# Kernel tuning notes

Hardware: AMD Instinct MI355X
Metric: run time of the kernel (lower is better)

## Reference

```python
import jax, jax.numpy as jnp
import numpy as np

N = 524288      # total nodes
B = 4096        # number of graphs (segments)
D = 128         # input_dim
H = 256         # nb_hidden


def setup_inputs() -> dict:
    key = jax.random.key(0)
    ks = jax.random.split(key, 10)
    X = jax.random.normal(ks[0], (N, D), jnp.float32)
    # sorted, contiguous, non-empty segment ids (pyg `batch` vector)
    batch = ((jnp.arange(N) * B) // N).astype(jnp.int32)
    s = 0.05
    W0 = jax.random.normal(ks[1], (D, H), jnp.float32) * s
    b0 = jnp.zeros((H,), jnp.float32)
    W1 = jax.random.normal(ks[2], (H, H), jnp.float32) * s
    b1 = jnp.zeros((H,), jnp.float32)
    W2 = jax.random.normal(ks[3], (H, H), jnp.float32) * s
    b2 = jnp.zeros((H,), jnp.float32)
    Wf = jax.random.normal(ks[4], (H, 1), jnp.float32) * s
    bf = jnp.zeros((1,), jnp.float32)
    return {"X": X, "W0": W0, "b0": b0, "W1": W1, "b1": b1,
            "W2": W2, "b2": b2, "Wf": Wf, "bf": bf, "batch": batch}


def reference(X, W0, b0, W1, b1, W2, b2, Wf, bf, batch):
    # MLP logits (nb_layers=3 hidden Linear+ReLU, then final Linear to 1)
    h = jax.nn.relu(X @ W0 + b0)
    h = jax.nn.relu(h @ W1 + b1)
    h = jax.nn.relu(h @ W2 + b2)
    logits = (h @ Wf + bf)[:, 0]                          # [N]

    # batched_softmax: exp -> segment add -> gather -> div (as in original)
    e = jnp.exp(logits)
    seg_sum = jax.ops.segment_sum(e, batch, num_segments=B)   # [B]
    probs = e / seg_sum[batch]                                # [N]

    # batched_sample: per-segment categorical sample via Gumbel-max
    skey = jax.random.key(42)
    u = jax.random.uniform(skey, (N,), jnp.float32, 1e-20, 1.0)
    g = -jnp.log(-jnp.log(u))
    score = jnp.log(probs) + g                                # [N]
    seg_max = jax.ops.segment_max(score, batch, num_segments=B)
    winner = jnp.where(score >= seg_max[batch], jnp.arange(N), -1)
    shifted_actions = jax.ops.segment_max(winner, batch, num_segments=B)  # global idx per segment [B]
    p = probs[shifted_actions]                                # [B]

    # get_batch_shift: start offset of each segment
    counts = jax.ops.segment_sum(jnp.ones((N,), jnp.int32), batch, num_segments=B)
    starts = jnp.concatenate([jnp.zeros((1,), jnp.int32), jnp.cumsum(counts)[:-1]])
    actions = shifted_actions - starts                        # [B] local index within graph
    return (p, actions, shifted_actions)
```

## Files before the change

kernel.cpp:

```cpp
#include <hip/hip_runtime.h>
#include <hip/hip_bf16.h>


#define NFULL 524288
#define BSEG  4096
#define SEGSZ 128
#define DIN   128
#define HID   256
#define MROWS 128
#define KPAD  264

typedef __bf16 bf16x8 __attribute__((ext_vector_type(8)));
typedef float  f32x4  __attribute__((ext_vector_type(4)));

__device__ __forceinline__ unsigned short f2bf(float f) {
  __hip_bfloat16 h = __float2bfloat16(f);
  return __builtin_bit_cast(unsigned short, h);
}

__global__ __launch_bounds__(256) void convert_weights(
    const float* __restrict__ W0, const float* __restrict__ W1,
    const float* __restrict__ W2,
    unsigned short* __restrict__ W0t, unsigned short* __restrict__ W1t,
    unsigned short* __restrict__ W2t) {
  const int tid = blockIdx.x * 256 + threadIdx.x;
  if (tid < 32768) {
    const int n = tid >> 7, k = tid & 127;
    W0t[tid] = f2bf(W0[k * 256 + n]);
  } else if (tid < 98304) {
    const int u = tid - 32768;
    const int n = u >> 8, k = u & 255;
    W1t[u] = f2bf(W1[k * 256 + n]);
  } else if (tid < 163840) {
    const int u = tid - 98304;
    const int n = u >> 8, k = u & 255;
    W2t[u] = f2bf(W2[k * 256 + n]);
  }
}


template<int K>
__device__ __forceinline__ void do_layer(
    const unsigned short* Abuf, const unsigned short* __restrict__ Wt,
    const float* __restrict__ bias, int wq, int wr, int lane,
    f32x4 (&acc)[4][4]) {
  const int l15 = lane & 15;
  const int q   = lane >> 4;
  #pragma unroll
  for (int ct = 0; ct < 4; ++ct) {
    const float4 bv4 = *(const float4*)&bias[wq * 64 + ct * 16 + q * 4];
    f32x4 c; c[0] = bv4.x; c[1] = bv4.y; c[2] = bv4.z; c[3] = bv4.w;
    #pragma unroll
    for (int rt = 0; rt < 4; ++rt) acc[ct][rt] = c;
  }
  const unsigned short* Wb = Wt + (wq * 64 + l15) * K + q * 8;
  const unsigned short* Ab = Abuf + (wr * 64 + l15) * KPAD + q * 8;
  #pragma unroll 2
  for (int k0 = 0; k0 < K; k0 += 32) {
    bf16x8 wv[4], rv[4];
    #pragma unroll
    for (int ct = 0; ct < 4; ++ct)
      wv[ct] = *(const bf16x8*)(Wb + ct * 16 * K + k0);
    #pragma unroll
    for (int rt = 0; rt < 4; ++rt)
      rv[rt] = *(const bf16x8*)(Ab + rt * 16 * KPAD + k0);
    #pragma unroll
    for (int ct = 0; ct < 4; ++ct)
      #pragma unroll
      for (int rt = 0; rt < 4; ++rt)
        acc[ct][rt] = __builtin_amdgcn_mfma_f32_16x16x32_bf16(
            wv[ct], rv[rt], acc[ct][rt], 0, 0, 0);
  }
}

__device__ __forceinline__ void writeback_relu(
    unsigned short* Abuf, int wq, int wr, int lane, const f32x4 (&acc)[4][4]) {
  const int l15 = lane & 15, q = lane >> 4;
  #pragma unroll
  for (int rt = 0; rt < 4; ++rt) {
    const int row = wr * 64 + rt * 16 + l15;
    #pragma unroll
    for (int ct = 0; ct < 4; ++ct) {
      const int col = wq * 64 + ct * 16 + q * 4;
      ushort4 p;
      p.x = f2bf(fmaxf(acc[ct][rt][0], 0.f));
      p.y = f2bf(fmaxf(acc[ct][rt][1], 0.f));
      p.z = f2bf(fmaxf(acc[ct][rt][2], 0.f));
      p.w = f2bf(fmaxf(acc[ct][rt][3], 0.f));
      *(ushort4*)&Abuf[row * KPAD + col] = p;
    }
  }
}

__device__ __forceinline__ void threefry2x32_42(unsigned x0, unsigned x1,
                                                unsigned& o0, unsigned& o1) {
  const unsigned ks0 = 0u, ks1 = 42u;
  const unsigned ks2 = ks0 ^ ks1 ^ 0x1BD11BDAu;
  x0 += ks0; x1 += ks1;
#define TF_R(r) { x0 += x1; x1 = (x1 << (r)) | (x1 >> (32 - (r))); x1 ^= x0; }
  TF_R(13) TF_R(15) TF_R(26) TF_R(6)   x0 += ks1; x1 += ks2 + 1u;
  TF_R(17) TF_R(29) TF_R(16) TF_R(24)  x0 += ks2; x1 += ks0 + 2u;
  TF_R(13) TF_R(15) TF_R(26) TF_R(6)   x0 += ks0; x1 += ks1 + 3u;
  TF_R(17) TF_R(29) TF_R(16) TF_R(24)  x0 += ks1; x1 += ks2 + 4u;
  TF_R(13) TF_R(15) TF_R(26) TF_R(6)   x0 += ks2; x1 += ks0 + 5u;
#undef TF_R
  o0 = x0; o1 = x1;
}

__global__ __launch_bounds__(512, 4) void mlp_fused(
    const float* __restrict__ X,
    const unsigned short* __restrict__ W0t,
    const unsigned short* __restrict__ W1t,
    const unsigned short* __restrict__ W2t,
    const float* __restrict__ b0, const float* __restrict__ b1,
    const float* __restrict__ b2,
    const float* __restrict__ Wf, const float* __restrict__ bfp,
    float* __restrict__ out) {
  __shared__ alignas(16) unsigned short Abuf[MROWS * KPAD];
  __shared__ float WfS[HID];
  __shared__ float Lpart[8][64];
  __shared__ float logit_sh[MROWS];
  __shared__ float red[2];
  __shared__ float smax_sh[2];
  __shared__ int   sidx_sh[2];
  const int tid  = threadIdx.x;
  const int lane = tid & 63;
  const int w    = tid >> 6;
  const int wq   = w & 3;
  const int wr   = w >> 2;
  const int l15  = lane & 15;
  const int q    = lane >> 4;
  const int seg  = blockIdx.x;
  const size_t row0 = (size_t)seg * MROWS;

  if (tid < HID) WfS[tid] = Wf[tid];

  #pragma unroll
  for (int it = 0; it < 8; ++it) {
    const int idx = tid + it * 512;
    const int r   = idx >> 5;
    const int k4  = (idx & 31) * 4;
    const float4 v = *(const float4*)&X[(row0 + r) * DIN + k4];
    ushort4 p;
    p.x = f2bf(v.x); p.y = f2bf(v.y); p.z = f2bf(v.z); p.w = f2bf(v.w);
    *(ushort4*)&Abuf[r * KPAD + k4] = p;
  }
  __syncthreads();

  f32x4 acc[4][4];
  do_layer<DIN>(Abuf, W0t, b0, wq, wr, lane, acc);
  __syncthreads();
  writeback_relu(Abuf, wq, wr, lane, acc);
  __syncthreads();
  do_layer<HID>(Abuf, W1t, b1, wq, wr, lane, acc);
  __syncthreads();
  writeback_relu(Abuf, wq, wr, lane, acc);
  __syncthreads();
  do_layer<HID>(Abuf, W2t, b2, wq, wr, lane, acc);

  {
    float part[4];
    #pragma unroll
    for (int rt = 0; rt < 4; ++rt) {
      float p = 0.f;
      #pragma unroll
      for (int ct = 0; ct < 4; ++ct) {
        const int col = wq * 64 + ct * 16 + q * 4;
        #pragma unroll
        for (int r = 0; r < 4; ++r)
          p = fmaf(fmaxf(acc[ct][rt][r], 0.f), WfS[col + r], p);
      }
      part[rt] = p;
    }
    #pragma unroll
    for (int rt = 0; rt < 4; ++rt) {
      part[rt] += __shfl_xor(part[rt], 16, 64);
      part[rt] += __shfl_xor(part[rt], 32, 64);
    }
    if (q == 0)
      #pragma unroll
      for (int rt = 0; rt < 4; ++rt) Lpart[w][rt * 16 + l15] = part[rt];
  }
  __syncthreads();
  if (tid < MROWS) {
    const int g = (tid >> 6) * 4;
    const int r = tid & 63;
    logit_sh[tid] = Lpart[g][r] + Lpart[g + 1][r] + Lpart[g + 2][r] +
                    Lpart[g + 3][r] + bfp[0];
  }
  __syncthreads();

  float e = 0.f, score = 0.f, prob = 0.f;
  if (tid < SEGSZ) {
    e = expf(logit_sh[tid]);
    float v = e;
    #pragma unroll
    for (int off = 32; off >= 1; off >>= 1) v += __shfl_xor(v, off, 64);
    if ((tid & 63) == 0) red[tid >> 6] = v;
  }
  __syncthreads();
  if (tid < SEGSZ) {
    const float S = red[0] + red[1];
    prob = e / S;
    unsigned o0, o1;
    threefry2x32_42(0u, (unsigned)(row0 + tid), o0, o1);
    const float f = __uint_as_float(0x3f800000u | (o0 >> 9)) - 1.0f;
    const float u = fmaxf(1e-20f, f + 1e-20f);
    const float g = -logf(-logf(u));
    score = logf(prob) + g;
    logit_sh[tid] = prob;
    float ms = score; int mi = tid;
    #pragma unroll
    for (int off = 1; off < 64; off <<= 1) {
      const float os = __shfl_xor(ms, off, 64);
      const int   oi = __shfl_xor(mi, off, 64);
      if (os > ms || (os == ms && oi > mi)) { ms = os; mi = oi; }
    }
    if ((tid & 63) == 0) { smax_sh[tid >> 6] = ms; sidx_sh[tid >> 6] = mi; }
  }
  __syncthreads();
  if (tid == 0) {
    const float s0 = smax_sh[0], s1 = smax_sh[1];
    const int   i0 = sidx_sh[0], i1 = sidx_sh[1];
    const int win = (s1 > s0 || (s1 == s0 && i1 > i0)) ? i1 : i0;
    out[seg]            = logit_sh[win];
    out[BSEG + seg]     = (float)win;
    out[2 * BSEG + seg] = (float)(row0 + win);
  }
}

extern "C" void kernel_launch(void* const* d_in, const int* in_sizes, int n_in,
                              void* d_out, int out_size, void* d_ws, size_t ws_size,
                              hipStream_t stream) {
  const float* X  = (const float*)d_in[0];
  const float* W0 = (const float*)d_in[1];
  const float* b0 = (const float*)d_in[2];
  const float* W1 = (const float*)d_in[3];
  const float* b1 = (const float*)d_in[4];
  const float* W2 = (const float*)d_in[5];
  const float* b2 = (const float*)d_in[6];
  const float* Wf = (const float*)d_in[7];
  const float* bf = (const float*)d_in[8];

  unsigned short* W0t = (unsigned short*)d_ws;
  unsigned short* W1t = W0t + 256 * 128;
  unsigned short* W2t = W1t + 256 * 256;
  float* out = (float*)d_out;

  convert_weights<<<640, 256, 0, stream>>>(W0, W1, W2, W0t, W1t, W2t);
  mlp_fused<<<BSEG, 512, 0, stream>>>(X, W0t, W1t, W2t, b0, b1, b2,
                                      Wf, bf, out);
}
```

Before: 656.4 us.

## Use 4 waves per block with 128x64 warp tiles and coalesced weight reads

The fused MLP kernel drops from 8 waves to 4 waves per 128-row block. Each wave now computes all 128 rows for a 64-column slice, so it holds 32 accumulators, and each weight fragment loaded from global memory feeds twice as many MFMAs. This cuts weight traffic through L2/global per block in half, at the cost of more registers per lane and fewer waves available to hide latency. The weight-conversion kernel also switches to coalesced reads with scattered writes.

```diff
diff --git a/kernel.cpp b/kernel.cpp
--- a/kernel.cpp
+++ b/kernel.cpp
@@ -25,16 +25,16 @@
     unsigned short* __restrict__ W2t) {
   const int tid = blockIdx.x * 256 + threadIdx.x;
   if (tid < 32768) {
-    const int n = tid >> 7, k = tid & 127;
-    W0t[tid] = f2bf(W0[k * 256 + n]);
+    const int k = tid >> 8, n = tid & 255;
+    W0t[n * 128 + k] = f2bf(W0[tid]);
   } else if (tid < 98304) {
     const int u = tid - 32768;
-    const int n = u >> 8, k = u & 255;
-    W1t[u] = f2bf(W1[k * 256 + n]);
+    const int k = u >> 8, n = u & 255;
+    W1t[n * 256 + k] = f2bf(W1[u]);
   } else if (tid < 163840) {
     const int u = tid - 98304;
-    const int n = u >> 8, k = u & 255;
-    W2t[u] = f2bf(W2[k * 256 + n]);
+    const int k = u >> 8, n = u & 255;
+    W2t[n * 256 + k] = f2bf(W2[u]);
   }
 }
 
@@ -42,46 +42,45 @@
 template<int K>
 __device__ __forceinline__ void do_layer(
     const unsigned short* Abuf, const unsigned short* __restrict__ Wt,
-    const float* __restrict__ bias, int wq, int wr, int lane,
-    f32x4 (&acc)[4][4]) {
+    const float* __restrict__ bias, int w, int lane, f32x4 (&acc)[4][8]) {
   const int l15 = lane & 15;
   const int q   = lane >> 4;
   #pragma unroll
   for (int ct = 0; ct < 4; ++ct) {
-    const float4 bv4 = *(const float4*)&bias[wq * 64 + ct * 16 + q * 4];
+    const float4 bv4 = *(const float4*)&bias[w * 64 + ct * 16 + q * 4];
     f32x4 c; c[0] = bv4.x; c[1] = bv4.y; c[2] = bv4.z; c[3] = bv4.w;
     #pragma unroll
-    for (int rt = 0; rt < 4; ++rt) acc[ct][rt] = c;
-  }
-  const unsigned short* Wb = Wt + (wq * 64 + l15) * K + q * 8;
-  const unsigned short* Ab = Abuf + (wr * 64 + l15) * KPAD + q * 8;
+    for (int rt = 0; rt < 8; ++rt) acc[ct][rt] = c;
+  }
+  const unsigned short* Wb = Wt + (w * 64 + l15) * K + q * 8;
+  const unsigned short* Ab = Abuf + l15 * KPAD + q * 8;
   #pragma unroll 2
   for (int k0 = 0; k0 < K; k0 += 32) {
-    bf16x8 wv[4], rv[4];
+    bf16x8 wv[4], rv[8];
     #pragma unroll
     for (int ct = 0; ct < 4; ++ct)
       wv[ct] = *(const bf16x8*)(Wb + ct * 16 * K + k0);
     #pragma unroll
-    for (int rt = 0; rt < 4; ++rt)
+    for (int rt = 0; rt < 8; ++rt)
       rv[rt] = *(const bf16x8*)(Ab + rt * 16 * KPAD + k0);
     #pragma unroll
     for (int ct = 0; ct < 4; ++ct)
       #pragma unroll
-      for (int rt = 0; rt < 4; ++rt)
+      for (int rt = 0; rt < 8; ++rt)
         acc[ct][rt] = __builtin_amdgcn_mfma_f32_16x16x32_bf16(
             wv[ct], rv[rt], acc[ct][rt], 0, 0, 0);
   }
 }
 
 __device__ __forceinline__ void writeback_relu(
-    unsigned short* Abuf, int wq, int wr, int lane, const f32x4 (&acc)[4][4]) {
+    unsigned short* Abuf, int w, int lane, const f32x4 (&acc)[4][8]) {
   const int l15 = lane & 15, q = lane >> 4;
   #pragma unroll
-  for (int rt = 0; rt < 4; ++rt) {
-    const int row = wr * 64 + rt * 16 + l15;
+  for (int rt = 0; rt < 8; ++rt) {
+    const int row = rt * 16 + l15;
     #pragma unroll
     for (int ct = 0; ct < 4; ++ct) {
-      const int col = wq * 64 + ct * 16 + q * 4;
+      const int col = w * 64 + ct * 16 + q * 4;
       ushort4 p;
       p.x = f2bf(fmaxf(acc[ct][rt][0], 0.f));
       p.y = f2bf(fmaxf(acc[ct][rt][1], 0.f));
@@ -107,7 +106,7 @@
   o0 = x0; o1 = x1;
 }
 
-__global__ __launch_bounds__(512, 4) void mlp_fused(
+__global__ __launch_bounds__(256, 2) void mlp_fused(
     const float* __restrict__ X,
     const unsigned short* __restrict__ W0t,
     const unsigned short* __restrict__ W1t,
@@ -118,7 +117,7 @@
     float* __restrict__ out) {
   __shared__ alignas(16) unsigned short Abuf[MROWS * KPAD];
   __shared__ float WfS[HID];
-  __shared__ float Lpart[8][64];
+  __shared__ float Lpart[4][MROWS];
   __shared__ float logit_sh[MROWS];
   __shared__ float red[2];
   __shared__ float smax_sh[2];
@@ -126,46 +125,45 @@
   const int tid  = threadIdx.x;
   const int lane = tid & 63;
   const int w    = tid >> 6;
-  const int wq   = w & 3;
-  const int wr   = w >> 2;
   const int l15  = lane & 15;
   const int q    = lane >> 4;
   const int seg  = blockIdx.x;
   const size_t row0 = (size_t)seg * MROWS;
 
-  if (tid < HID) WfS[tid] = Wf[tid];
-
-  #pragma unroll
-  for (int it = 0; it < 8; ++it) {
-    const int idx = tid + it * 512;
-    const int r   = idx >> 5;
-    const int k4  = (idx & 31) * 4;
-    const float4 v = *(const float4*)&X[(row0 + r) * DIN + k4];
-    ushort4 p;
-    p.x = f2bf(v.x); p.y = f2bf(v.y); p.z = f2bf(v.z); p.w = f2bf(v.w);
-    *(ushort4*)&Abuf[r * KPAD + k4] = p;
-  }
-  __syncthreads();
-
-  f32x4 acc[4][4];
-  do_layer<DIN>(Abuf, W0t, b0, wq, wr, lane, acc);
-  __syncthreads();
-  writeback_relu(Abuf, wq, wr, lane, acc);
-  __syncthreads();
-  do_layer<HID>(Abuf, W1t, b1, wq, wr, lane, acc);
-  __syncthreads();
-  writeback_relu(Abuf, wq, wr, lane, acc);
-  __syncthreads();
-  do_layer<HID>(Abuf, W2t, b2, wq, wr, lane, acc);
+  WfS[tid] = Wf[tid];
 
   {
-    float part[4];
-    #pragma unroll
-    for (int rt = 0; rt < 4; ++rt) {
+    const int k4 = (tid & 31) * 4;
+    int r = tid >> 5;
+    #pragma unroll
+    for (int it = 0; it < 16; ++it, r += 8) {
+      const float4 v = *(const float4*)&X[(row0 + r) * DIN + k4];
+      ushort4 p;
+      p.x = f2bf(v.x); p.y = f2bf(v.y); p.z = f2bf(v.z); p.w = f2bf(v.w);
+      *(ushort4*)&Abuf[r * KPAD + k4] = p;
+    }
+  }
+  __syncthreads();
+
+  f32x4 acc[4][8];
+  do_layer<DIN>(Abuf, W0t, b0, w, lane, acc);
+  __syncthreads();
+  writeback_relu(Abuf, w, lane, acc);
+  __syncthreads();
+  do_layer<HID>(Abuf, W1t, b1, w, lane, acc);
+  __syncthreads();
+  writeback_relu(Abuf, w, lane, acc);
+  __syncthreads();
+  do_layer<HID>(Abuf, W2t, b2, w, lane, acc);
+
+  {
+    float part[8];
+    #pragma unroll
+    for (int rt = 0; rt < 8; ++rt) {
       float p = 0.f;
       #pragma unroll
       for (int ct = 0; ct < 4; ++ct) {
-        const int col = wq * 64 + ct * 16 + q * 4;
+        const int col = w * 64 + ct * 16 + q * 4;
         #pragma unroll
         for (int r = 0; r < 4; ++r)
           p = fmaf(fmaxf(acc[ct][rt][r], 0.f), WfS[col + r], p);
@@ -173,24 +171,21 @@
       part[rt] = p;
     }
     #pragma unroll
-    for (int rt = 0; rt < 4; ++rt) {
+    for (int rt = 0; rt < 8; ++rt) {
       part[rt] += __shfl_xor(part[rt], 16, 64);
       part[rt] += __shfl_xor(part[rt], 32, 64);
     }
     if (q == 0)
       #pragma unroll
-      for (int rt = 0; rt < 4; ++rt) Lpart[w][rt * 16 + l15] = part[rt];
-  }
-  __syncthreads();
-  if (tid < MROWS) {
-    const int g = (tid >> 6) * 4;
-    const int r = tid & 63;
-    logit_sh[tid] = Lpart[g][r] + Lpart[g + 1][r] + Lpart[g + 2][r] +
-                    Lpart[g + 3][r] + bfp[0];
-  }
-  __syncthreads();
-
-  float e = 0.f, score = 0.f, prob = 0.f;
+      for (int rt = 0; rt < 8; ++rt) Lpart[w][rt * 16 + l15] = part[rt];
+  }
+  __syncthreads();
+  if (tid < MROWS)
+    logit_sh[tid] = Lpart[0][tid] + Lpart[1][tid] + Lpart[2][tid] +
+                    Lpart[3][tid] + bfp[0];
+  __syncthreads();
+
+  float e = 0.f, prob = 0.f;
   if (tid < SEGSZ) {
     e = expf(logit_sh[tid]);
     float v = e;
@@ -207,7 +202,7 @@
     const float f = __uint_as_float(0x3f800000u | (o0 >> 9)) - 1.0f;
     const float u = fmaxf(1e-20f, f + 1e-20f);
     const float g = -logf(-logf(u));
-    score = logf(prob) + g;
+    const float score = logf(prob) + g;
     logit_sh[tid] = prob;
     float ms = score; int mi = tid;
     #pragma unroll
@@ -248,6 +243,6 @@
   float* out = (float*)d_out;
 
   convert_weights<<<640, 256, 0, stream>>>(W0, W1, W2, W0t, W1t, W2t);
-  mlp_fused<<<BSEG, 512, 0, stream>>>(X, W0t, W1t, W2t, b0, b1, b2,
+  mlp_fused<<<BSEG, 256, 0, stream>>>(X, W0t, W1t, W2t, b0, b1, b2,
                                       Wf, bf, out);
 }
```

Result: faster. 534.0 us (-18.7%).
